# Performance work log

Hardware: AMD Instinct MI355X
Metric: run time of the kernel (lower is better)

## Reference

```python
import jax, jax.numpy as jnp
import numpy as np

RADIUS = 4  # matches init_kwargs
EPS = 1e-12  # torch F.normalize eps


def _l2_normalize(x):
    # normalize over channel dim (axis=1), matching F.normalize(p=2, dim=1)
    n = jnp.sqrt(jnp.sum(x * x, axis=1, keepdims=True))
    return x / jnp.maximum(n, EPS)


def setup_inputs() -> dict:
    key = jax.random.key(0)
    k1, k2 = jax.random.split(key)
    B, C, H, W = 8, 256, 128, 192
    return {
        "feat1": jax.random.normal(k1, (B, C, H, W), dtype=jnp.float32),
        "feat2": jax.random.normal(k2, (B, C, H, W), dtype=jnp.float32),
    }


def reference(feat1, feat2):
    r = RADIUS
    B, C, H, W = feat1.shape
    f1 = _l2_normalize(feat1)
    f2 = _l2_normalize(feat2)
    f2p = jnp.pad(f2, ((0, 0), (0, 0), (r, r), (r, r)))  # [B,C,H+2r,W+2r]
    # fixed (2r+1)^2 = 81 static offsets; loop is over offsets, not data dims
    corrs = []
    for dy in range(-r, r + 1):
        for dx in range(-r, r + 1):
            shifted = f2p[:, :, dy + r:dy + r + H, dx + r:dx + r + W]
            corrs.append(jnp.sum(f1 * shifted, axis=1))  # [B,H,W]
    return jnp.stack(corrs, axis=1)  # [B,(2r+1)^2,H,W]
```

## Files before the change

### kernel.cpp

```cpp
#include <hip/hip_runtime.h>
#include <math.h>

namespace {

constexpr int B_ = 8, C_ = 256, H_ = 128, W_ = 192;
constexpr int HW = H_ * W_;
constexpr size_t CHW = (size_t)C_ * HW;
constexpr int TH = 8, TW = 16;
constexpr int NTHREADS = 512;
constexpr int KCH = 16;
constexpr int NCHUNK = C_ / KCH;
constexpr int BROWS = 16;
constexpr int BPOS = 32;
constexpr int POSB = 48;
constexpr int ROWB = BPOS * POSB;
constexpr int BUFB = BROWS * ROWB;
constexpr int OSTR = 20;
constexpr int OUTB = 81 * 4 * OSTR * 4;
constexpr int BNOFF = OUTB;
constexpr int LDSB = BNOFF + BROWS * BPOS * 4;

typedef _Float16 f16x4 __attribute__((ext_vector_type(4)));
typedef _Float16 f16x8 __attribute__((ext_vector_type(8)));
typedef float f32x4 __attribute__((ext_vector_type(4)));
typedef _Float16 h2 __attribute__((ext_vector_type(2)));

__device__ __forceinline__ unsigned pk2(float x, float y) {
    return __builtin_bit_cast(unsigned, __builtin_amdgcn_cvt_pkrtz(x, y));
}
__device__ __forceinline__ float dot2f(unsigned a, unsigned b, float c) {
#if __has_builtin(__builtin_amdgcn_fdot2)
    return __builtin_amdgcn_fdot2(__builtin_bit_cast(h2, a),
                                  __builtin_bit_cast(h2, b), c, false);
#else
    const h2 ha = __builtin_bit_cast(h2, a), hb = __builtin_bit_cast(h2, b);
    return fmaf((float)ha.x, (float)hb.x, fmaf((float)ha.y, (float)hb.y, c));
#endif
}
__device__ __forceinline__ f32x4 mfma16(f16x4 a, f16x4 b, f32x4 c) {
#if __has_builtin(__builtin_amdgcn_mfma_f32_16x16x16f16)
    return __builtin_amdgcn_mfma_f32_16x16x16f16(a, b, c, 0, 0, 0);
#else
    const f16x8 a8 = {a[0], a[1], a[2], a[3], (_Float16)0, (_Float16)0, (_Float16)0, (_Float16)0};
    const f16x8 b8 = {b[0], b[1], b[2], b[3], (_Float16)0, (_Float16)0, (_Float16)0, (_Float16)0};
    return __builtin_amdgcn_mfma_f32_16x16x32_f16(a8, b8, c, 0, 0, 0);
#endif
}

__global__ __launch_bounds__(NTHREADS)
void local_corr_mfma(const float* __restrict__ f1g,
                     const float* __restrict__ f2g,
                     float* __restrict__ outg)
{
    __shared__ __align__(16) char lds[LDSB];

    const int m  = blockIdx.x;
    const int b  = m & 7;
    const int k  = m >> 3;
    const int bx = k % 12;
    const int by = k / 12;
    const int w0 = bx * TW, h0 = by * TH;

    const int tid  = threadIdx.x;
    const int hs   = tid >> 6;
    const int lane = tid & 63;
    const int lp   = lane & 15;
    const int lg   = lane >> 4;

    const int sr = tid >> 5;
    const int sc = tid & 31;
    const int bgh = h0 - 4 + sr, bgw = w0 - 8 + sc;
    const bool bok = (bgh >= 0) && (bgh < H_) && (bgw >= 0) && (bgw < W_);
    const int bghc = min(max(bgh, 0), H_ - 1);
    const int bgwc = min(max(bgw, 0), W_ - 1);
    const float* bptr = f2g + (size_t)b * CHW + (size_t)bghc * W_ + bgwc;
    const float* aptr = f1g + (size_t)b * CHW + (size_t)(h0 + hs) * W_ + (w0 + lp)
                            + (size_t)(4 * lg) * HW;

    float bvr[16], avr[4];
    float bn = 0.f, an = 0.f;
    f16x4 afrag;

    auto issue = [&]() {
#pragma unroll
        for (int j = 0; j < 16; ++j) bvr[j] = bptr[(size_t)j * HW];
#pragma unroll
        for (int j = 0; j < 4; ++j) avr[j] = aptr[(size_t)j * HW];
        bptr += (size_t)KCH * HW;
        aptr += (size_t)KCH * HW;
    };

    auto stage = [&]() {
        unsigned u[8];
#pragma unroll
        for (int q = 0; q < 8; ++q) {
            const float x = bok ? bvr[2 * q] : 0.f;
            const float y = bok ? bvr[2 * q + 1] : 0.f;
            u[q] = pk2(x, y);
            bn = dot2f(u[q], u[q], bn);
        }
        char* dst = lds + tid * POSB;
        *reinterpret_cast<uint4*>(dst)      = make_uint4(u[0], u[1], u[2], u[3]);
        *reinterpret_cast<uint4*>(dst + 16) = make_uint4(u[4], u[5], u[6], u[7]);
        const unsigned a0 = pk2(avr[0], avr[1]);
        const unsigned a1 = pk2(avr[2], avr[3]);
        an = dot2f(a0, a0, an);
        an = dot2f(a1, a1, an);
        afrag = __builtin_bit_cast(f16x4, make_uint2(a0, a1));
    };

    f32x4 acc[9][2];
#pragma unroll
    for (int dy = 0; dy < 9; ++dy)
#pragma unroll
        for (int bt = 0; bt < 2; ++bt) acc[dy][bt] = (f32x4)0.f;

    const int fro = lp * POSB + lg * 8;

    auto compute = [&]() {
#pragma unroll
        for (int dy = 0; dy < 9; ++dy) {
            const char* rbase = lds + (hs + dy) * ROWB + fro;
            const f16x4 b0 = *reinterpret_cast<const f16x4*>(rbase);
            const f16x4 b1 = *reinterpret_cast<const f16x4*>(rbase + 16 * POSB);
            acc[dy][0] = mfma16(afrag, b0, acc[dy][0]);
            acc[dy][1] = mfma16(afrag, b1, acc[dy][1]);
        }
    };

    issue();
    stage();
    __syncthreads();
    for (int t = 0; t < NCHUNK; ++t) {
        const bool more = (t + 1) < NCHUNK;
        if (more) issue();
        compute();
        __syncthreads();
        if (more) stage();
        __syncthreads();
    }

    float* bnorm = reinterpret_cast<float*>(lds + BNOFF);
    bnorm[tid] = bn;
    an += __shfl_xor(an, 16);
    an += __shfl_xor(an, 32);
    const float inv1own = 1.0f / fmaxf(sqrtf(an), 1e-12f);
    __syncthreads();

    const size_t obase = (size_t)b * 81 * HW;
#pragma unroll
    for (int pass = 0; pass < 2; ++pass) {
        if ((hs >> 2) == pass) {
            const int h4 = hs & 3;
#pragma unroll
            for (int dy = 0; dy < 9; ++dy) {
#pragma unroll
                for (int bt = 0; bt < 2; ++bt) {
                    const int scol = bt * 16 + lp;
                    const float nb = bnorm[(hs + dy) * 32 + scol];
                    const float v2 = 1.0f / fmaxf(sqrtf(nb), 1e-12f);
#pragma unroll
                    for (int r = 0; r < 4; ++r) {
                        const int mw  = 4 * lg + r;
                        const int dxi = scol - 4 - mw;
                        const float v1 = __shfl(inv1own, mw);
                        if (dxi >= 0 && dxi <= 8) {
                            float* orow = reinterpret_cast<float*>(lds)
                                        + ((dy * 9 + dxi) * 4 + h4) * OSTR;
                            orow[mw] = acc[dy][bt][r] * v1 * v2;
                        }
                    }
                }
            }
        }
        __syncthreads();
        for (int s = tid; s < 81 * 4 * 4; s += NTHREADS) {
            const int od = s >> 4;
            const int rem = s & 15;
            const int h4 = rem >> 2, q = rem & 3;
            const float4 v = *reinterpret_cast<const float4*>(
                reinterpret_cast<const float*>(lds) + (od * 4 + h4) * OSTR + q * 4);
            *reinterpret_cast<float4*>(outg + obase + (size_t)od * HW +
                                       (size_t)(h0 + pass * 4 + h4) * W_ + w0 + q * 4) = v;
        }
        if (pass == 0) __syncthreads();
    }
}

}

extern "C" void kernel_launch(void* const* d_in, const int* in_sizes, int n_in,
                              void* d_out, int out_size, void* d_ws, size_t ws_size,
                              hipStream_t stream)
{
    (void)in_sizes; (void)n_in; (void)d_ws; (void)ws_size; (void)out_size;
    const float* f1 = (const float*)d_in[0];
    const float* f2 = (const float*)d_in[1];
    float* out = (float*)d_out;

    dim3 grid(1536, 1, 1);
    dim3 block(NTHREADS);
    local_corr_mfma<<<grid, block, 0, stream>>>(f1, f2, out);
}
```

Before: 172.7 us.

## Double-buffer LDS tiles and vectorize feat2 loads as float2 pairs

Feat2 staging now uses two LDS buffers, so the main loop computes on one while packing the next chunk into the other. This halves the number of block barriers per channel chunk. Each thread now loads two adjacent pixels over 8 channels with float2 loads instead of one pixel over 16 scalar channels. It keeps per-half partial norms and sums them in the epilogue, and it keeps two register sets of prefetched loads in flight. The cost is about 48KB of LDS per block instead of about 28KB, plus more registers, which may lower occupancy.

```diff
diff --git a/kernel.cpp b/kernel.cpp
--- a/kernel.cpp
+++ b/kernel.cpp
@@ -17,8 +17,8 @@
 constexpr int BUFB = BROWS * ROWB;
 constexpr int OSTR = 20;
 constexpr int OUTB = 81 * 4 * OSTR * 4;
-constexpr int BNOFF = OUTB;
-constexpr int LDSB = BNOFF + BROWS * BPOS * 4;
+constexpr int BN2OFF = OUTB;
+constexpr int LDSB = 2 * BUFB;
 
 typedef _Float16 f16x4 __attribute__((ext_vector_type(4)));
 typedef _Float16 f16x8 __attribute__((ext_vector_type(8)));
@@ -67,43 +67,51 @@
     const int lp   = lane & 15;
     const int lg   = lane >> 4;
 
-    const int sr = tid >> 5;
-    const int sc = tid & 31;
-    const int bgh = h0 - 4 + sr, bgw = w0 - 8 + sc;
-    const bool bok = (bgh >= 0) && (bgh < H_) && (bgw >= 0) && (bgw < W_);
-    const int bghc = min(max(bgh, 0), H_ - 1);
-    const int bgwc = min(max(bgw, 0), W_ - 1);
-    const float* bptr = f2g + (size_t)b * CHW + (size_t)bghc * W_ + bgwc;
-    const float* aptr = f1g + (size_t)b * CHW + (size_t)(h0 + hs) * W_ + (w0 + lp)
-                            + (size_t)(4 * lg) * HW;
-
-    float bvr[16], avr[4];
-    float bn = 0.f, an = 0.f;
+    const int half = tid & 1;
+    const int sc2  = (tid >> 1) & 15;
+    const int sr   = tid >> 5;
+    const int gh   = h0 - 4 + sr;
+    const int gw0  = w0 - 8 + 2 * sc2;
+    const bool rok = (gh >= 0) && (gh < H_);
+    const unsigned msk0 = (rok && gw0 >= 0 && gw0 < W_) ? 0xFFFFFFFFu : 0u;
+    const unsigned msk1 = (rok && gw0 + 1 >= 0 && gw0 + 1 < W_) ? 0xFFFFFFFFu : 0u;
+    const int bghc = min(max(gh, 0), H_ - 1);
+    const int bgwc = min(max(gw0, 0), W_ - 2);
+    const float* bbase = f2g + (size_t)b * CHW + (size_t)bghc * W_ + bgwc
+                             + (size_t)(8 * half) * HW;
+    const float* abase = f1g + (size_t)b * CHW + (size_t)(h0 + hs) * W_ + (w0 + lp)
+                             + (size_t)(4 * lg) * HW;
+    const int swoff = sr * ROWB + (2 * sc2) * POSB + half * 16;
+
+    float2 bv0[8], bv1[8];
+    float av0[4], av1[4];
+    float bn0 = 0.f, bn1 = 0.f, an = 0.f;
     f16x4 afrag;
 
-    auto issue = [&]() {
-#pragma unroll
-        for (int j = 0; j < 16; ++j) bvr[j] = bptr[(size_t)j * HW];
-#pragma unroll
-        for (int j = 0; j < 4; ++j) avr[j] = aptr[(size_t)j * HW];
-        bptr += (size_t)KCH * HW;
-        aptr += (size_t)KCH * HW;
+    auto issueLd = [&](int c0, float2* bv, float* av) {
+        const float* bp = bbase + (size_t)c0 * HW;
+#pragma unroll
+        for (int j = 0; j < 8; ++j)
+            bv[j] = *reinterpret_cast<const float2*>(bp + (size_t)j * HW);
+        const float* ap = abase + (size_t)c0 * HW;
+#pragma unroll
+        for (int j = 0; j < 4; ++j) av[j] = ap[(size_t)j * HW];
     };
 
-    auto stage = [&]() {
-        unsigned u[8];
-#pragma unroll
-        for (int q = 0; q < 8; ++q) {
-            const float x = bok ? bvr[2 * q] : 0.f;
-            const float y = bok ? bvr[2 * q + 1] : 0.f;
-            u[q] = pk2(x, y);
-            bn = dot2f(u[q], u[q], bn);
-        }
-        char* dst = lds + tid * POSB;
-        *reinterpret_cast<uint4*>(dst)      = make_uint4(u[0], u[1], u[2], u[3]);
-        *reinterpret_cast<uint4*>(dst + 16) = make_uint4(u[4], u[5], u[6], u[7]);
-        const unsigned a0 = pk2(avr[0], avr[1]);
-        const unsigned a1 = pk2(avr[2], avr[3]);
+    auto stageF = [&](int buf, const float2* bv, const float* av) {
+        unsigned u0[4], u1[4];
+#pragma unroll
+        for (int q = 0; q < 4; ++q) {
+            u0[q] = pk2(bv[2 * q].x, bv[2 * q + 1].x) & msk0;
+            u1[q] = pk2(bv[2 * q].y, bv[2 * q + 1].y) & msk1;
+            bn0 = dot2f(u0[q], u0[q], bn0);
+            bn1 = dot2f(u1[q], u1[q], bn1);
+        }
+        char* dst = lds + buf * BUFB + swoff;
+        *reinterpret_cast<uint4*>(dst)        = make_uint4(u0[0], u0[1], u0[2], u0[3]);
+        *reinterpret_cast<uint4*>(dst + POSB) = make_uint4(u1[0], u1[1], u1[2], u1[3]);
+        const unsigned a0 = pk2(av[0], av[1]);
+        const unsigned a1 = pk2(av[2], av[3]);
         an = dot2f(a0, a0, an);
         an = dot2f(a1, a1, an);
         afrag = __builtin_bit_cast(f16x4, make_uint2(a0, a1));
@@ -117,10 +125,10 @@
 
     const int fro = lp * POSB + lg * 8;
 
-    auto compute = [&]() {
+    auto computeF = [&](int buf) {
 #pragma unroll
         for (int dy = 0; dy < 9; ++dy) {
-            const char* rbase = lds + (hs + dy) * ROWB + fro;
+            const char* rbase = lds + buf * BUFB + (hs + dy) * ROWB + fro;
             const f16x4 b0 = *reinterpret_cast<const f16x4*>(rbase);
             const f16x4 b1 = *reinterpret_cast<const f16x4*>(rbase + 16 * POSB);
             acc[dy][0] = mfma16(afrag, b0, acc[dy][0]);
@@ -128,20 +136,24 @@
         }
     };
 
-    issue();
-    stage();
+    issueLd(0, bv0, av0);
+    stageF(0, bv0, av0);
+    issueLd(KCH, bv1, av1);
     __syncthreads();
-    for (int t = 0; t < NCHUNK; ++t) {
-        const bool more = (t + 1) < NCHUNK;
-        if (more) issue();
-        compute();
+    for (int t = 0; t < NCHUNK; t += 2) {
+        if (t + 2 < NCHUNK) issueLd((t + 2) * KCH, bv0, av0);
+        computeF(0);
+        stageF(1, bv1, av1);
         __syncthreads();
-        if (more) stage();
+        if (t + 3 < NCHUNK) issueLd((t + 3) * KCH, bv1, av1);
+        computeF(1);
+        if (t + 2 < NCHUNK) stageF(0, bv0, av0);
         __syncthreads();
     }
 
-    float* bnorm = reinterpret_cast<float*>(lds + BNOFF);
-    bnorm[tid] = bn;
+    float* bn2 = reinterpret_cast<float*>(lds + BN2OFF);
+    bn2[(sr * 32 + 2 * sc2) * 2 + half]     = bn0;
+    bn2[(sr * 32 + 2 * sc2 + 1) * 2 + half] = bn1;
     an += __shfl_xor(an, 16);
     an += __shfl_xor(an, 32);
     const float inv1own = 1.0f / fmaxf(sqrtf(an), 1e-12f);
@@ -157,8 +169,9 @@
 #pragma unroll
                 for (int bt = 0; bt < 2; ++bt) {
                     const int scol = bt * 16 + lp;
-                    const float nb = bnorm[(hs + dy) * 32 + scol];
-                    const float v2 = 1.0f / fmaxf(sqrtf(nb), 1e-12f);
+                    const float2 nb = *reinterpret_cast<const float2*>(
+                        bn2 + ((hs + dy) * 32 + scol) * 2);
+                    const float v2 = 1.0f / fmaxf(sqrtf(nb.x + nb.y), 1e-12f);
 #pragma unroll
                     for (int r = 0; r < 4; ++r) {
                         const int mw  = 4 * lg + r;
```

Measured after the change: 260.9 us. 51.1% more time.
